# Performance work log

Measured on AMD Instinct MI355X. Metric: run time of the kernel, lower is better.

The kernel has to match this reference:

```python
import jax, jax.numpy as jnp
import numpy as np

PI = float(np.pi)
N_BINS_POT = 140
TIMESTEP = 0.02
ATOMS = ["N", "CA", "C", "cent"]
ANGLES = [("N", "CA", "C", 0), ("CA", "C", "N", 1), ("C", "N", "CA", 2), ("N", "CA", "cent", 0), ("C", "CA", "cent", 0)]
DIHEDRALS = [("C", "N", "CA", "C", 3), ("N", "CA", "C", "N", 1), ("CA", "C", "N", "CA", 2), ("C", "N", "CA", "cent", 3), ("cent", "CA", "C", "N", 1)]

_gap_ang = (PI - PI / 3) / N_BINS_POT
ANGLE_CENTRES = np.array([PI / 3 + i * _gap_ang + 0.5 * _gap_ang for i in range(N_BINS_POT)][1:-1], dtype=np.float32)  # 138
_gap_dih = 2 * PI / N_BINS_POT
DIH_CENTRES = np.array([-PI + i * _gap_dih - 0.5 * _gap_dih for i in range(N_BINS_POT + 2)][1:-1], dtype=np.float32)  # 140


def safe_norm(v, axis=-1, keepdims=False):
    sq = jnp.sum(v * v, axis=axis, keepdims=keepdims)
    return jnp.where(sq > 0, jnp.sqrt(jnp.where(sq > 0, sq, 1.0)), 0.0)


def normalize(v):
    # torch.nn.functional.normalize with eps=1e-12
    return v / jnp.maximum(safe_norm(v, keepdims=True), 1e-12)


def _gather_force(pots, inds):
    # pots: [n, n_bins]; inds: [b, n] -> 0.5 * (pots[r, i] - pots[r, i+2])
    r = jnp.arange(pots.shape[0])[None, :]
    return 0.5 * (pots[r, inds] - pots[r, inds + 2])


def _accelerations(coords, masses, pair_centres, pair_pots, angle_pots, dih_pots):
    b, n_atoms, _ = coords.shape
    n_res = n_atoms // 4
    # ---- all-pairs distance forces (bin by argmin against per-pair centres, gather) ----
    diffs = coords[:, None, :, :] - coords[:, :, None, :]  # [b, i, j, 3] = c[j] - c[i]
    dists = safe_norm(diffs)  # [b, i, j]
    df = dists.reshape(b, n_atoms * n_atoms)
    inds = jnp.argmin(jnp.abs(pair_centres[None] - df[:, :, None]), axis=2)  # [b, n^2]
    pair_forces = _gather_force(pair_pots, inds).reshape(b, n_atoms, n_atoms)
    norm_diffs = diffs / jnp.maximum(dists, 0.01)[..., None]
    accs = jnp.sum(pair_forces[..., None] * norm_diffs, axis=1) / masses[..., None]
    # ---- bond-angle forces ----
    ac = coords.reshape(b, n_res, 4, 3)
    aa = jnp.zeros_like(ac)
    ang_centres = jnp.asarray(ANGLE_CENTRES)
    for ai, (a1, a2, a3, across) in enumerate(ANGLES):
        i1, i2, i3 = ATOMS.index(a1), ATOMS.index(a2), ATOMS.index(a3)
        if across == 0:
            ba = ac[:, :, i1] - ac[:, :, i2]; bc = ac[:, :, i3] - ac[:, :, i2]; pots = angle_pots[ai]
        elif across == 1:
            ba = ac[:, :-1, i1] - ac[:, :-1, i2]; bc = ac[:, 1:, i3] - ac[:, :-1, i2]; pots = angle_pots[ai][:-1]
        else:
            ba = ac[:, :-1, i1] - ac[:, 1:, i2]; bc = ac[:, 1:, i3] - ac[:, 1:, i2]; pots = angle_pots[ai][1:]
        ban = safe_norm(ba); bcn = safe_norm(bc)
        angs = jnp.arccos(jnp.sum(ba * bc, axis=2) / (ban * bcn))
        ainds = jnp.argmin(jnp.abs(ang_centres[None, None] - angs[:, :, None]), axis=2)
        f = _gather_force(pots, ainds)[..., None]
        cr = jnp.cross(ba, bc)
        fa = f * normalize(jnp.cross(ba, cr)) / ban[..., None]
        fc = f * normalize(jnp.cross(-bc, cr)) / bcn[..., None]
        fb = -fa - fc
        if across == 0:
            aa = aa.at[:, :, i1].add(fa).at[:, :, i2].add(fb).at[:, :, i3].add(fc)
        elif across == 1:
            aa = aa.at[:, :-1, i1].add(fa).at[:, :-1, i2].add(fb).at[:, 1:, i3].add(fc)
        else:
            aa = aa.at[:, :-1, i1].add(fa).at[:, 1:, i2].add(fb).at[:, 1:, i3].add(fc)
    # ---- dihedral forces ----
    dih_centres = jnp.asarray(DIH_CENTRES)
    for di, (a1, a2, a3, a4, across) in enumerate(DIHEDRALS):
        i1, i2, i3, i4 = ATOMS.index(a1), ATOMS.index(a2), ATOMS.index(a3), ATOMS.index(a4)
        if across == 1:
            ab = ac[:, :-1, i2] - ac[:, :-1, i1]; bc = ac[:, :-1, i3] - ac[:, :-1, i2]; cd = ac[:, 1:, i4] - ac[:, :-1, i3]
            pots = dih_pots[di][:-1]
        elif across == 2:
            ab = ac[:, :-1, i2] - ac[:, :-1, i1]; bc = ac[:, 1:, i3] - ac[:, :-1, i2]; cd = ac[:, 1:, i4] - ac[:, 1:, i3]
            pots = dih_pots[di][1:]
        else:  # across == 3
            ab = ac[:, 1:, i2] - ac[:, :-1, i1]; bc = ac[:, 1:, i3] - ac[:, 1:, i2]; cd = ac[:, 1:, i4] - ac[:, 1:, i3]
            pots = dih_pots[di][1:]
        c1 = jnp.cross(ab, bc); c2 = jnp.cross(bc, cd)
        bcn = safe_norm(bc, keepdims=True)
        dihs = jnp.arctan2(jnp.sum(jnp.cross(c1, c2) * bc / bcn, axis=2), jnp.sum(c1 * c2, axis=2))
        dinds = jnp.argmin(jnp.abs(dih_centres[None, None] - dihs[:, :, None]), axis=2)
        f = _gather_force(pots, dinds)[..., None]
        fa = f * normalize(-c1) / safe_norm(ab, keepdims=True)
        fd = f * normalize(c2) / safe_norm(cd, keepdims=True)
        bsq = jnp.squeeze(bcn, -1) ** 2
        t1 = (jnp.sum(ab * bc, axis=2) / bsq)[..., None]
        t2 = (jnp.sum(cd * bc, axis=2) / bsq)[..., None]
        fb = -fa - t1 * fa + t2 * fd  # torque-balancing middle-atom forces
        fc = -fa - fb - fd
        if across == 1:
            aa = aa.at[:, :-1, i1].add(fa).at[:, :-1, i2].add(fb).at[:, :-1, i3].add(fc).at[:, 1:, i4].add(fd)
        elif across == 2:
            aa = aa.at[:, :-1, i1].add(fa).at[:, :-1, i2].add(fb).at[:, 1:, i3].add(fc).at[:, 1:, i4].add(fd)
        else:
            aa = aa.at[:, :-1, i1].add(fa).at[:, 1:, i2].add(fb).at[:, 1:, i3].add(fc).at[:, 1:, i4].add(fd)
    return accs + aa.reshape(b, n_atoms, 3) / masses[..., None]


def _simulate(coords, vels, masses, ff_distances, ff_angles, ff_dihedrals,
              dist_bin_centres, inters_flat, inters_ang, inters_dih, n_steps):
    pair_centres = dist_bin_centres[inters_flat]  # [n^2, 138]
    pair_pots = ff_distances[inters_flat]         # [n^2, 140]
    angle_pots = ff_angles[:, inters_ang]         # [5, n_res, 140]
    dih_pots = ff_dihedrals[:, inters_dih]        # [5, n_res, 142]

    def step(carry, _):
        c, v, a_last = carry
        c = c + v * TIMESTEP + 0.5 * a_last * TIMESTEP * TIMESTEP
        a = _accelerations(c, masses, pair_centres, pair_pots, angle_pots, dih_pots)
        v = v + 0.5 * (a_last + a) * TIMESTEP
        return (c, v, a), None

    (coords, vels, _), _ = jax.lax.scan(step, (coords, vels, jnp.zeros_like(coords)), None, length=n_steps)
    return coords


def setup_inputs() -> dict:
    key = jax.random.key(0)
    ks = jax.random.split(key, 10)
    b, n_res = 1, 100
    n_atoms = n_res * 4
    n2 = n_atoms * n_atoms
    n_dist_types = 4000
    coords = jax.random.normal(ks[0], (b, n_atoms, 3), jnp.float32) * 10.0
    vels = jax.random.normal(ks[1], (b, n_atoms, 3), jnp.float32) * 0.1  # start_temperature = 0.1
    masses = jax.random.uniform(ks[2], (b, n_atoms), jnp.float32, 0.5, 1.5)
    native_coords = jax.random.normal(ks[3], (b, n_atoms, 3), jnp.float32) * 10.0
    ff_distances = jax.random.normal(ks[4], (n_dist_types, 140), jnp.float32) * 0.1
    ff_angles = jax.random.normal(ks[5], (5, 20, 140), jnp.float32) * 0.1
    ff_dihedrals = jax.random.normal(ks[6], (5, 20, 142), jnp.float32) * 0.1
    centres = jnp.linspace(1.0, 15.9, 138, dtype=jnp.float32)
    dist_bin_centres = jnp.tile(centres[None, :], (n_dist_types, 1))
    inters_flat = jax.random.randint(ks[7], (n2,), 0, n_dist_types)
    inters_ang = jax.random.randint(ks[8], (n_res,), 0, 20)
    inters_dih = jax.random.randint(ks[9], (n_res,), 0, 20)
    return {"coords": coords, "vels": vels, "masses": masses, "native_coords": native_coords,
            "ff_distances": ff_distances, "ff_angles": ff_angles, "ff_dihedrals": ff_dihedrals,
            "dist_bin_centres": dist_bin_centres, "inters_flat": inters_flat,
            "inters_ang": inters_ang, "inters_dih": inters_dih, "n_steps": 3}


def reference(coords, vels, masses, native_coords, ff_distances, ff_angles, ff_dihedrals,
              dist_bin_centres, inters_flat, inters_ang, inters_dih, n_steps):
    # native_coords is only used for RMSD reporting in the original; it does not affect the dynamics.
    return _simulate(coords, vels, masses, ff_distances, ff_angles, ff_dihedrals,
                     dist_bin_centres, inters_flat, inters_ang, inters_dih, n_steps)
```

## Files before the change

kernel.cpp:

```cpp
#include <hip/hip_runtime.h>
#include <math.h>

#define N_ATOMS 400
#define N_RES   100
#define DT      0.02f
#define PI_D    3.14159265358979323846
#define NBLK    100
#define NTHR    256

struct V3 { float x, y, z; };
__device__ __forceinline__ V3 v3(float x, float y, float z) { V3 r{x,y,z}; return r; }
__device__ __forceinline__ V3 sub(V3 a, V3 b) { return v3(a.x-b.x, a.y-b.y, a.z-b.z); }
__device__ __forceinline__ V3 neg(V3 a) { return v3(-a.x, -a.y, -a.z); }
__device__ __forceinline__ V3 scale(V3 a, float s) { return v3(a.x*s, a.y*s, a.z*s); }
__device__ __forceinline__ float dot3(V3 a, V3 b) { return a.x*b.x + a.y*b.y + a.z*b.z; }
__device__ __forceinline__ V3 cross3(V3 a, V3 b) {
    return v3(a.y*b.z - a.z*b.y, a.z*b.x - a.x*b.z, a.x*b.y - a.y*b.x);
}
__device__ __forceinline__ float vnorm(V3 a) {
    float s = dot3(a, a);
    return s > 0.0f ? sqrtf(s) : 0.0f;
}
__device__ __forceinline__ V3 normalize3(V3 a) {
    float n = fmaxf(vnorm(a), 1e-12f);
    return scale(a, 1.0f/n);
}

__device__ __forceinline__ int clampi(int i, int lo, int hi) {
    return i < lo ? lo : (i > hi ? hi : i);
}
__device__ __forceinline__ int bin_dist(float d) {
    const float INV = (float)(137.0/14.9);
    return clampi((int)floorf((d - 1.0f)*INV + 0.5f), 0, 137);
}
__device__ __forceinline__ int bin_ang(float a) {
    const float C0  = (float)(PI_D/3.0 + 1.5*((PI_D - PI_D/3.0)/140.0));
    const float INV = (float)(140.0/(PI_D - PI_D/3.0));
    return clampi((int)floorf((a - C0)*INV + 0.5f), 0, 137);
}
__device__ __forceinline__ int bin_dih(float a) {
    const float C0  = (float)(-PI_D + 0.5*(2.0*PI_D/140.0));
    const float INV = (float)(140.0/(2.0*PI_D));
    return clampi((int)floorf((a - C0)*INV + 0.5f), 0, 139);
}

__constant__ int ANG_I[5][3]   = {{0,1,2},{1,2,0},{2,0,1},{0,1,3},{2,1,3}};
__constant__ int ANG_ACROSS[5] = {0,1,2,0,0};
__constant__ int DIH_I[5][4]   = {{2,0,1,2},{0,1,2,0},{1,2,0,1},{2,0,1,3},{3,1,2,0}};
__constant__ int DIH_ACROSS[5] = {3,1,2,3,1};

__device__ __forceinline__ V3 ldpos(const float* c, int res, int atom) {
    int k = (res*4 + atom)*3;
    return v3(c[k], c[k+1], c[k+2]);
}

__device__ __forceinline__ void addOwn(float* sF, int b, int res, int atom, V3 f) {
    if (res == b) {
        atomicAdd(&sF[atom*3+0], f.x);
        atomicAdd(&sF[atom*3+1], f.y);
        atomicAdd(&sF[atom*3+2], f.z);
    }
}

__device__ __forceinline__ void bonded_own(int u, int b, const float* sc,
                              const float* __restrict__ ffa, const float* __restrict__ ffdih,
                              const int* __restrict__ ia, const int* __restrict__ idh,
                              float* sF) {
    int e = u % 10, which = u / 10;
    int r = b - which;
    if (e < 5) {
        int across = ANG_ACROSS[e];
        bool valid = which ? (b >= 1 && across != 0)
                           : (across == 0 || b <= N_RES-2);
        if (!valid) return;
        int i1 = ANG_I[e][0], i2 = ANG_I[e][1], i3 = ANG_I[e][2];
        int o2 = (across == 2) ? 1 : 0;
        int o3 = (across != 0) ? 1 : 0;
        V3 p1 = ldpos(sc, r,     i1);
        V3 p2 = ldpos(sc, r+o2,  i2);
        V3 p3 = ldpos(sc, r+o3,  i3);
        V3 ba = sub(p1, p2);
        V3 bc = sub(p3, p2);
        float ban = vnorm(ba), bcn = vnorm(bc);
        float ca = dot3(ba, bc) / (ban*bcn);
        ca = fminf(1.0f, fmaxf(-1.0f, ca));
        float ang = acosf(ca);
        int ind = bin_ang(ang);
        int potr = (across == 2) ? r+1 : r;
        const float* row = ffa + (e*20 + ia[potr])*140;
        float f = 0.5f*(row[ind] - row[ind+2]);
        V3 cr = cross3(ba, bc);
        V3 fa = scale(normalize3(cross3(ba, cr)), f/ban);
        V3 fc = scale(normalize3(neg(cross3(bc, cr))), f/bcn);
        V3 fb = neg(v3(fa.x+fc.x, fa.y+fc.y, fa.z+fc.z));
        addOwn(sF, b, r,     i1, fa);
        addOwn(sF, b, r+o2,  i2, fb);
        addOwn(sF, b, r+o3,  i3, fc);
    } else {
        int di = e - 5;
        bool valid = which ? (b >= 1) : (b <= N_RES-2);
        if (!valid) return;
        int across = DIH_ACROSS[di];
        int i1 = DIH_I[di][0], i2 = DIH_I[di][1], i3 = DIH_I[di][2], i4 = DIH_I[di][3];
        int o2 = (across == 3) ? 1 : 0;
        int o3 = (across >= 2) ? 1 : 0;
        int o4 = 1;
        V3 p1 = ldpos(sc, r,     i1);
        V3 p2 = ldpos(sc, r+o2,  i2);
        V3 p3 = ldpos(sc, r+o3,  i3);
        V3 p4 = ldpos(sc, r+o4,  i4);
        V3 ab = sub(p2, p1);
        V3 bc = sub(p3, p2);
        V3 cd = sub(p4, p3);
        V3 c1 = cross3(ab, bc);
        V3 c2 = cross3(bc, cd);
        float bcn = vnorm(bc);
        V3 cc = cross3(c1, c2);
        float y = dot3(cc, bc) / bcn;
        float x = dot3(c1, c2);
        float dih = atan2f(y, x);
        int ind = bin_dih(dih);
        int potr = (across == 1) ? r : r+1;
        const float* row = ffdih + (di*20 + idh[potr])*142;
        float f = 0.5f*(row[ind] - row[ind+2]);
        V3 fa = scale(normalize3(neg(c1)), f / vnorm(ab));
        V3 fd = scale(normalize3(c2),      f / vnorm(cd));
        float bsq = bcn*bcn;
        float t1 = dot3(ab, bc)/bsq;
        float t2 = dot3(cd, bc)/bsq;
        V3 fb = v3(-fa.x - t1*fa.x + t2*fd.x,
                   -fa.y - t1*fa.y + t2*fd.y,
                   -fa.z - t1*fa.z + t2*fd.z);
        V3 fc = v3(-fa.x - fb.x - fd.x,
                   -fa.y - fb.y - fd.y,
                   -fa.z - fb.z - fd.z);
        addOwn(sF, b, r,     i1, fa);
        addOwn(sF, b, r+o2,  i2, fb);
        addOwn(sF, b, r+o3,  i3, fc);
        addOwn(sF, b, r+o4,  i4, fd);
    }
}

__device__ __forceinline__ void force_phase(int b, int tid, int lane, int wave,
                              const float* sc, float* sF, const int* ty,
                              const float* __restrict__ ffd, const float* __restrict__ ffa,
                              const float* __restrict__ ffdih, const int* __restrict__ ia,
                              const int* __restrict__ idh) {
    if (tid < 20) bonded_own(tid, b, sc, ffa, ffdih, ia, idh, sF);

    int j = b*4 + wave;
    float cx = sc[3*j], cy = sc[3*j+1], cz = sc[3*j+2];
    float fx = 0.0f, fy = 0.0f, fz = 0.0f;
    #pragma unroll
    for (int k = 0; k < 7; ++k) {
        int i = lane + 64*k;
        if (k < 6 || i < N_ATOMS) {
            float dx = cx - sc[3*i];
            float dy = cy - sc[3*i+1];
            float dz = cz - sc[3*i+2];
            float d2 = dx*dx + dy*dy + dz*dz;
            float d  = d2 > 0.0f ? sqrtf(d2) : 0.0f;
            int ind  = bin_dist(d);
            const float* row = ffd + ty[k]*140;
            float f = 0.5f*(row[ind] - row[ind+2]);
            float w = f / fmaxf(d, 0.01f);
            fx += w*dx; fy += w*dy; fz += w*dz;
        }
    }
    #pragma unroll
    for (int off = 32; off > 0; off >>= 1) {
        fx += __shfl_down(fx, off);
        fy += __shfl_down(fy, off);
        fz += __shfl_down(fz, off);
    }
    if (lane == 0) {
        atomicAdd(&sF[wave*3+0], fx);
        atomicAdd(&sF[wave*3+1], fy);
        atomicAdd(&sF[wave*3+2], fz);
    }
}

__global__ void __launch_bounds__(NTHR)
stepA(const float* __restrict__ cin, const float* __restrict__ vin,
      const float* __restrict__ masses, const float* __restrict__ ffd,
      const float* __restrict__ ffa, const float* __restrict__ ffdih,
      const int* __restrict__ iflat, const int* __restrict__ ia,
      const int* __restrict__ idh, float* __restrict__ c2,
      float* __restrict__ v1, float* __restrict__ a1)
{
    __shared__ float sc[N_ATOMS*3];
    __shared__ float sF[12];
    const int tid  = threadIdx.x;
    const int b    = blockIdx.x;
    const int lane = tid & 63;
    const int wave = tid >> 6;
    const int j    = b*4 + wave;

    int ty[7];
    #pragma unroll
    for (int k = 0; k < 7; ++k) {
        int i = lane + 64*k;
        ty[k] = (k < 6 || i < N_ATOMS) ? iflat[i*N_ATOMS + j] : 0;
    }

    for (int q = tid; q < 300; q += NTHR) {
        float4 cv = ((const float4*)cin)[q];
        float4 vv = ((const float4*)vin)[q];
        float4 r;
        r.x = cv.x + vv.x*DT; r.y = cv.y + vv.y*DT;
        r.z = cv.z + vv.z*DT; r.w = cv.w + vv.w*DT;
        ((float4*)sc)[q] = r;
    }
    if (tid < 12) sF[tid] = 0.0f;
    __syncthreads();

    force_phase(b, tid, lane, wave, sc, sF, ty, ffd, ffa, ffdih, ia, idh);
    __syncthreads();

    if (tid < 12) {
        int t = b*12 + tid;
        float a = sF[tid] / masses[b*4 + tid/3];
        float v = vin[t] + 0.5f*a*DT;
        float cc = sc[t] + v*DT + 0.5f*a*DT*DT;
        c2[t] = cc; v1[t] = v; a1[t] = a;
    }
}

__global__ void __launch_bounds__(NTHR)
stepB(const float* __restrict__ masses, const float* __restrict__ ffd,
      const float* __restrict__ ffa, const float* __restrict__ ffdih,
      const int* __restrict__ iflat, const int* __restrict__ ia,
      const int* __restrict__ idh, const float* __restrict__ c2,
      const float* __restrict__ v1, const float* __restrict__ a1,
      float* __restrict__ out)
{
    __shared__ float sc[N_ATOMS*3];
    __shared__ float sF[12];
    const int tid  = threadIdx.x;
    const int b    = blockIdx.x;
    const int lane = tid & 63;
    const int wave = tid >> 6;
    const int j    = b*4 + wave;

    int ty[7];
    #pragma unroll
    for (int k = 0; k < 7; ++k) {
        int i = lane + 64*k;
        ty[k] = (k < 6 || i < N_ATOMS) ? iflat[i*N_ATOMS + j] : 0;
    }

    for (int q = tid; q < 300; q += NTHR)
        ((float4*)sc)[q] = ((const float4*)c2)[q];
    if (tid < 12) sF[tid] = 0.0f;
    __syncthreads();

    force_phase(b, tid, lane, wave, sc, sF, ty, ffd, ffa, ffdih, ia, idh);
    __syncthreads();

    if (tid < 12) {
        int t = b*12 + tid;
        float a = sF[tid] / masses[b*4 + tid/3];
        float v = v1[t] + 0.5f*(a1[t] + a)*DT;
        out[t] = sc[t] + v*DT + 0.5f*a*DT*DT;
    }
}

extern "C" void kernel_launch(void* const* d_in, const int* in_sizes, int n_in,
                              void* d_out, int out_size, void* d_ws, size_t ws_size,
                              hipStream_t stream) {
    const float* coords = (const float*)d_in[0];
    const float* vels   = (const float*)d_in[1];
    const float* masses = (const float*)d_in[2];
    const float* ffd    = (const float*)d_in[4];
    const float* ffa    = (const float*)d_in[5];
    const float* ffdih  = (const float*)d_in[6];
    const int* iflat    = (const int*)d_in[8];
    const int* ia       = (const int*)d_in[9];
    const int* idh      = (const int*)d_in[10];
    float* out = (float*)d_out;

    float* ws = (float*)d_ws;
    float* c2 = ws;
    float* v1 = ws + 1200;
    float* a1 = ws + 2400;

    stepA<<<NBLK, NTHR, 0, stream>>>(coords, vels, masses, ffd, ffa, ffdih,
                                     iflat, ia, idh, c2, v1, a1);
    stepB<<<NBLK, NTHR, 0, stream>>>(masses, ffd, ffa, ffdih,
                                     iflat, ia, idh, c2, v1, a1, out);
}
```

Measured before the change: 92.71 us.

## Fuse both integration steps into one kernel with a global grid barrier

Merges stepA and stepB into a single kernel. A software grid-wide barrier, an atomic epoch counter with spin-wait, sits between the two force phases. Per-atom velocity, acceleration and mass stay in registers and the interaction-type loads are reused, which removes the second kernel launch and the workspace round trip for v1/a1. The barrier assumes all 100 blocks are co-resident. It also has a bounded spin that could break out early and read stale data.

```diff
diff --git a/kernel.cpp b/kernel.cpp
--- a/kernel.cpp
+++ b/kernel.cpp
@@ -7,6 +7,8 @@
 #define PI_D    3.14159265358979323846
 #define NBLK    100
 #define NTHR    256
+
+__device__ unsigned long long g_epoch = 0ULL;
 
 struct V3 { float x, y, z; };
 __device__ __forceinline__ V3 v3(float x, float y, float z) { V3 r{x,y,z}; return r; }
@@ -181,12 +183,12 @@
 }
 
 __global__ void __launch_bounds__(NTHR)
-stepA(const float* __restrict__ cin, const float* __restrict__ vin,
-      const float* __restrict__ masses, const float* __restrict__ ffd,
-      const float* __restrict__ ffa, const float* __restrict__ ffdih,
-      const int* __restrict__ iflat, const int* __restrict__ ia,
-      const int* __restrict__ idh, float* __restrict__ c2,
-      float* __restrict__ v1, float* __restrict__ a1)
+sim_fused(const float* __restrict__ cin, const float* __restrict__ vin,
+          const float* __restrict__ masses, const float* __restrict__ ffd,
+          const float* __restrict__ ffa, const float* __restrict__ ffdih,
+          const int* __restrict__ iflat, const int* __restrict__ ia,
+          const int* __restrict__ idh, float* __restrict__ c2,
+          float* __restrict__ out)
 {
     __shared__ float sc[N_ATOMS*3];
     __shared__ float sF[12];
@@ -217,41 +219,35 @@
     force_phase(b, tid, lane, wave, sc, sF, ty, ffd, ffa, ffdih, ia, idh);
     __syncthreads();
 
+    float v1r = 0.0f, a1r = 0.0f, mr = 1.0f;
     if (tid < 12) {
         int t = b*12 + tid;
-        float a = sF[tid] / masses[b*4 + tid/3];
-        float v = vin[t] + 0.5f*a*DT;
-        float cc = sc[t] + v*DT + 0.5f*a*DT*DT;
-        c2[t] = cc; v1[t] = v; a1[t] = a;
-    }
-}
-
-__global__ void __launch_bounds__(NTHR)
-stepB(const float* __restrict__ masses, const float* __restrict__ ffd,
-      const float* __restrict__ ffa, const float* __restrict__ ffdih,
-      const int* __restrict__ iflat, const int* __restrict__ ia,
-      const int* __restrict__ idh, const float* __restrict__ c2,
-      const float* __restrict__ v1, const float* __restrict__ a1,
-      float* __restrict__ out)
-{
-    __shared__ float sc[N_ATOMS*3];
-    __shared__ float sF[12];
-    const int tid  = threadIdx.x;
-    const int b    = blockIdx.x;
-    const int lane = tid & 63;
-    const int wave = tid >> 6;
-    const int j    = b*4 + wave;
-
-    int ty[7];
-    #pragma unroll
-    for (int k = 0; k < 7; ++k) {
-        int i = lane + 64*k;
-        ty[k] = (k < 6 || i < N_ATOMS) ? iflat[i*N_ATOMS + j] : 0;
-    }
+        mr  = masses[b*4 + tid/3];
+        a1r = sF[tid] / mr;
+        v1r = vin[t] + 0.5f*a1r*DT;
+        float cc = sc[t] + v1r*DT + 0.5f*a1r*DT*DT;
+        c2[t] = cc;
+        sF[tid] = 0.0f;
+    }
+
+    __syncthreads();
+    if (tid == 0) {
+        __builtin_amdgcn_fence(__ATOMIC_RELEASE, "agent");
+        unsigned long long t = __hip_atomic_fetch_add(&g_epoch, 1ULL,
+                                  __ATOMIC_RELAXED, __HIP_MEMORY_SCOPE_AGENT);
+        unsigned long long target = (t/NBLK)*NBLK + NBLK;
+        long iters = 0;
+        while (__hip_atomic_load(&g_epoch, __ATOMIC_RELAXED,
+                                 __HIP_MEMORY_SCOPE_AGENT) < target) {
+            __builtin_amdgcn_s_sleep(1);
+            if (++iters > (1L << 24)) break;
+        }
+        __builtin_amdgcn_fence(__ATOMIC_ACQUIRE, "agent");
+    }
+    __syncthreads();
 
     for (int q = tid; q < 300; q += NTHR)
         ((float4*)sc)[q] = ((const float4*)c2)[q];
-    if (tid < 12) sF[tid] = 0.0f;
     __syncthreads();
 
     force_phase(b, tid, lane, wave, sc, sF, ty, ffd, ffa, ffdih, ia, idh);
@@ -259,9 +255,9 @@
 
     if (tid < 12) {
         int t = b*12 + tid;
-        float a = sF[tid] / masses[b*4 + tid/3];
-        float v = v1[t] + 0.5f*(a1[t] + a)*DT;
-        out[t] = sc[t] + v*DT + 0.5f*a*DT*DT;
+        float a2 = sF[tid] / mr;
+        float v2 = v1r + 0.5f*(a1r + a2)*DT;
+        out[t] = sc[t] + v2*DT + 0.5f*a2*DT*DT;
     }
 }
 
@@ -279,13 +275,8 @@
     const int* idh      = (const int*)d_in[10];
     float* out = (float*)d_out;
 
-    float* ws = (float*)d_ws;
-    float* c2 = ws;
-    float* v1 = ws + 1200;
-    float* a1 = ws + 2400;
-
-    stepA<<<NBLK, NTHR, 0, stream>>>(coords, vels, masses, ffd, ffa, ffdih,
-                                     iflat, ia, idh, c2, v1, a1);
-    stepB<<<NBLK, NTHR, 0, stream>>>(masses, ffd, ffa, ffdih,
-                                     iflat, ia, idh, c2, v1, a1, out);
-}
+    float* c2 = (float*)d_ws;
+
+    sim_fused<<<NBLK, NTHR, 0, stream>>>(coords, vels, masses, ffd, ffa, ffdih,
+                                         iflat, ia, idh, c2, out);
+}
```

After: 94.41 us. Within noise of the previous version (+1.8%).
